# Kernel optimization log

Hardware: AMD Instinct MI355X
Metric: run time of the kernel (lower is better)

## Reference

```python
import jax, jax.numpy as jnp
import numpy as np

N_NODES = 25000
N_EDGES = 400000
FEAT = 128
HID = 64
HEADS = 4
NUM_CLASSES = 2
NUM_GRAPHS = 64


def setup_inputs() -> dict:
    key = jax.random.key(0)
    ks = jax.random.split(key, 16)
    x = jax.random.normal(ks[0], (N_NODES, FEAT), dtype=jnp.float32)
    edge_index = jax.random.randint(ks[1], (2, N_EDGES), 0, N_NODES, dtype=jnp.int32)
    batch = jnp.sort(jax.random.randint(ks[2], (N_NODES,), 0, NUM_GRAPHS, dtype=jnp.int32))
    s = 1.0 / np.sqrt(FEAT)
    sh = 1.0 / np.sqrt(HID)
    shc = 1.0 / np.sqrt(HID * HEADS)
    return {
        "x": x,
        "edge_index": edge_index,
        "batch": batch,
        # conv1: GraphConv(FEAT -> HID): lin_rel (bias) on aggregated neighbors + lin_root (no bias)
        "W1_rel": jax.random.uniform(ks[3], (FEAT, HID), jnp.float32, -s, s),
        "b1": jnp.zeros((HID,), jnp.float32),
        "W1_root": jax.random.uniform(ks[4], (FEAT, HID), jnp.float32, -s, s),
        # conv3: GATConv(HID -> HID, heads=HEADS), concat output [N, HEADS*HID]
        "Wg": jax.random.uniform(ks[5], (HID, HEADS * HID), jnp.float32, -sh, sh),
        "att_src": jax.random.uniform(ks[6], (HEADS, HID), jnp.float32, -sh, sh),
        "att_dst": jax.random.uniform(ks[7], (HEADS, HID), jnp.float32, -sh, sh),
        "bg": jnp.zeros((HEADS * HID,), jnp.float32),
        # conv5: GraphConv(HEADS*HID -> HID)
        "W5_rel": jax.random.uniform(ks[8], (HEADS * HID, HID), jnp.float32, -shc, shc),
        "b5": jnp.zeros((HID,), jnp.float32),
        "W5_root": jax.random.uniform(ks[9], (HEADS * HID, HID), jnp.float32, -shc, shc),
        # fc head
        "W_fc1": jax.random.uniform(ks[10], (HID, HID), jnp.float32, -sh, sh),
        "b_fc1": jnp.zeros((HID,), jnp.float32),
        "W_fc2": jax.random.uniform(ks[11], (HID, NUM_CLASSES), jnp.float32, -sh, sh),
        "b_fc2": jnp.zeros((NUM_CLASSES,), jnp.float32),
    }


def _graph_conv(h, src, dst, W_rel, b, W_root):
    # PyG GraphConv (aggr='add'): out_i = W_rel @ sum_{j->i} h_j + b + W_root @ h_i
    agg = jax.ops.segment_sum(h[src], dst, num_segments=N_NODES)
    return agg @ W_rel + b + h @ W_root


def _gat_conv(h, src, dst, Wg, att_src, att_dst, bg):
    # GATConv with default add_self_loops=True; eval mode (no attn dropout)
    n = h.shape[0]
    loop = jnp.arange(n, dtype=src.dtype)
    si = jnp.concatenate([src, loop])
    di = jnp.concatenate([dst, loop])
    xl = (h @ Wg).reshape(n, HEADS, HID)              # [N, H, C]
    a_s = jnp.sum(xl * att_src, axis=-1)              # [N, H]
    a_d = jnp.sum(xl * att_dst, axis=-1)              # [N, H]
    e = jax.nn.leaky_relu(a_s[si] + a_d[di], 0.2)     # [E', H]
    m = jax.ops.segment_max(e, di, num_segments=n)
    p = jnp.exp(e - m[di])
    denom = jax.ops.segment_sum(p, di, num_segments=n)
    alpha = p / denom[di]                             # segment softmax over incoming edges
    out = jax.ops.segment_sum(alpha[:, :, None] * xl[si], di, num_segments=n)
    return out.reshape(n, HEADS * HID) + bg


def reference(x, edge_index, batch, W1_rel, b1, W1_root, Wg, att_src, att_dst, bg,
              W5_rel, b5, W5_root, W_fc1, b_fc1, W_fc2, b_fc2):
    src, dst = edge_index[0], edge_index[1]
    h = jax.nn.relu(_graph_conv(x, src, dst, W1_rel, b1, W1_root))
    h = jax.nn.relu(_gat_conv(h, src, dst, Wg, att_src, att_dst, bg))
    h = jax.nn.relu(_graph_conv(h, src, dst, W5_rel, b5, W5_root))
    g = jax.ops.segment_sum(h, batch, num_segments=NUM_GRAPHS)   # global_add_pool
    g = jax.nn.relu(g @ W_fc1 + b_fc1)
    return jax.nn.sigmoid(g @ W_fc2 + b_fc2)
```

## Files before the change

### kernel.cpp

```cpp
#include <hip/hip_runtime.h>
#include <math.h>

#define N_NODES 25000
#define N_EDGES 400000
#define FEAT 128
#define HID 64
#define HEADS 4
#define HH 256
#define NUM_GRAPHS 64
#define BUCKET 96

typedef unsigned short ushort_t;
typedef unsigned int uint_t;
typedef __attribute__((ext_vector_type(8))) short short8;
typedef __attribute__((ext_vector_type(4))) float f32x4;

__device__ __forceinline__ float lrelu(float x){ return x > 0.f ? x : 0.2f*x; }

__device__ __forceinline__ ushort_t f2bf(float f){
  uint_t u = __float_as_uint(f);
  return (ushort_t)((u + 0x7fffu + ((u >> 16) & 1u)) >> 16);
}
#define BF_LO(u) __uint_as_float((u) << 16)
#define BF_HI(u) __uint_as_float((u) & 0xffff0000u)

__global__ __launch_bounds__(256) void conv1_gemm(
    const float* __restrict__ X, const float* __restrict__ Wrel,
    const float* __restrict__ Wroot, const float* __restrict__ bias,
    ushort_t* __restrict__ out_rel_b, float* __restrict__ out_root)
{
  const int w    = __builtin_amdgcn_readfirstlane(threadIdx.x >> 6);
  const int lane = threadIdx.x & 63;
  const int m = w >> 1, q = w & 1;
  const float* Wm = (m ? Wroot : Wrel) + (size_t)q*64*HID;
  float wreg[64];
  #pragma unroll
  for (int k = 0; k < 64; k++) wreg[k] = Wm[k*HID + lane];
  __shared__ float part[2][2][8][64];
  const int base = blockIdx.x*8;
  const float* __restrict__ xr = X + (size_t)base*FEAT + q*64;
  float acc[8] = {0,0,0,0,0,0,0,0};
  #pragma unroll
  for (int k = 0; k < 64; k++){
    const float wv = wreg[k];
    #pragma unroll
    for (int i = 0; i < 8; i++) acc[i] += xr[(size_t)i*FEAT + k]*wv;
  }
  #pragma unroll
  for (int i = 0; i < 8; i++) part[m][q][i][lane] = acc[i];
  __syncthreads();
  #pragma unroll
  for (int t = threadIdx.x; t < 1024; t += 256){
    int mm = t >> 9, ii = (t >> 6) & 7, cc = t & 63;
    float v = part[mm][0][ii][cc] + part[mm][1][ii][cc];
    if (mm) out_root[(size_t)(base+ii)*HID + cc] = v + bias[cc];
    else    out_rel_b[(size_t)(base+ii)*HID + cc] = f2bf(v);
  }
}

__global__ __launch_bounds__(512) void conv5_gemm(
    const float* __restrict__ X, const float* __restrict__ Wrel,
    const float* __restrict__ Wroot, const float* __restrict__ bias,
    ushort_t* __restrict__ out_rel_b, float* __restrict__ out_root)
{
  const int w    = __builtin_amdgcn_readfirstlane(threadIdx.x >> 6);
  const int lane = threadIdx.x & 63;
  const int m = w >> 2, q = w & 3;
  const float* Wm = (m ? Wroot : Wrel) + (size_t)q*64*HID;
  float wreg[64];
  #pragma unroll
  for (int k = 0; k < 64; k++) wreg[k] = Wm[k*HID + lane];
  __shared__ float part[2][4][8][64];
  const int base = blockIdx.x*8;
  const float* __restrict__ xr = X + (size_t)base*HH + q*64;
  float acc[8] = {0,0,0,0,0,0,0,0};
  #pragma unroll
  for (int k = 0; k < 64; k++){
    const float wv = wreg[k];
    #pragma unroll
    for (int i = 0; i < 8; i++) acc[i] += xr[(size_t)i*HH + k]*wv;
  }
  #pragma unroll
  for (int i = 0; i < 8; i++) part[m][q][i][lane] = acc[i];
  __syncthreads();
  #pragma unroll
  for (int t = threadIdx.x; t < 1024; t += 512){
    int mm = t >> 9, ii = (t >> 6) & 7, cc = t & 63;
    float v = part[mm][0][ii][cc] + part[mm][1][ii][cc]
            + part[mm][2][ii][cc] + part[mm][3][ii][cc];
    if (mm) out_root[(size_t)(base+ii)*HID + cc] = v + bias[cc];
    else    out_rel_b[(size_t)(base+ii)*HID + cc] = f2bf(v);
  }
}

__global__ __launch_bounds__(256) void k3_prep(
    const float* __restrict__ Wg, ushort_t* __restrict__ wgb)
{
  const int t = threadIdx.x;
  for (int i = 0; i < 64; i++){
    int e = t*64 + i;
    int j = e & 7, lane = (e >> 3) & 63, kt = (e >> 9) & 1, nt = e >> 10;
    int k = kt*32 + (lane >> 4)*8 + j;
    int n = nt*16 + (lane & 15);
    wgb[e] = f2bf(Wg[k*HH + n]);
  }
}

__global__ __launch_bounds__(256) void k3_mfma(
    const ushort_t* __restrict__ h1b, const ushort_t* __restrict__ wgb,
    const float* __restrict__ att_src, const float* __restrict__ att_dst,
    ushort_t* __restrict__ xlb, float* __restrict__ a_s, float* __restrict__ a_d)
{
  const int wid  = __builtin_amdgcn_readfirstlane(threadIdx.x >> 6);
  const int lane = threadIdx.x & 63;
  const int quad = lane >> 4, col = lane & 15;
  const int nb = blockIdx.x*64 + wid*16;
  const ushort_t* arow = h1b + (size_t)(nb + col)*HID + quad*8;
  short8 a0 = *(const short8*)(arow);
  short8 a1 = *(const short8*)(arow + 32);
  float as_acc[4] = {0,0,0,0}, ad_acc[4] = {0,0,0,0};
  #pragma unroll
  for (int nt = 0; nt < 16; nt++){
    short8 b0 = *(const short8*)(wgb + ((size_t)(nt*2+0)*64 + lane)*8);
    short8 b1 = *(const short8*)(wgb + ((size_t)(nt*2+1)*64 + lane)*8);
    f32x4 d = {0.f, 0.f, 0.f, 0.f};
    d = __builtin_amdgcn_mfma_f32_16x16x32_bf16(a0, b0, d, 0, 0, 0);
    d = __builtin_amdgcn_mfma_f32_16x16x32_bf16(a1, b1, d, 0, 0, 0);
    const int h = nt >> 2;
    const float asv = att_src[h*HID + (nt & 3)*16 + col];
    const float adv = att_dst[h*HID + (nt & 3)*16 + col];
    #pragma unroll
    for (int r = 0; r < 4; r++){
      const int node = nb + quad*4 + r;
      if (node < N_NODES)
        xlb[(size_t)node*HH + nt*16 + col] = f2bf(d[r]);
      as_acc[r] += d[r]*asv;
      ad_acc[r] += d[r]*adv;
    }
    if ((nt & 3) == 3){
      #pragma unroll
      for (int r = 0; r < 4; r++){
        float s1 = as_acc[r], s2 = ad_acc[r];
        #pragma unroll
        for (int off = 1; off < 16; off <<= 1){
          s1 += __shfl_xor(s1, off, 64);
          s2 += __shfl_xor(s2, off, 64);
        }
        const int node = nb + quad*4 + r;
        if (col == 0 && node < N_NODES){
          a_s[node*HEADS + h] = s1;
          a_d[node*HEADS + h] = s2;
        }
        as_acc[r] = 0.f; ad_acc[r] = 0.f;
      }
    }
  }
}

__global__ __launch_bounds__(256) void k_fill(const int* __restrict__ src,
                                              const int* __restrict__ dst,
                                              int* __restrict__ cnt,
                                              int* __restrict__ slot)
{
  int e = blockIdx.x*256 + threadIdx.x;
  if (e >= N_EDGES) return;
  int d = dst[e];
  int pos = atomicAdd(&cnt[d], 1);
  if (pos < BUCKET) slot[(size_t)d*BUCKET + pos] = src[e];
}

template<bool BF16OUT>
__global__ __launch_bounds__(256) void k_aggb(
    const int* __restrict__ cnt, const int* __restrict__ slot,
    const ushort_t* __restrict__ featb, const float* __restrict__ root,
    float* __restrict__ outf, ushort_t* __restrict__ outb)
{
  const int node = blockIdx.x*4 + (threadIdx.x >> 6);
  const int lane = threadIdx.x & 63;
  const int* __restrict__ sl = slot + (size_t)node*BUCKET;
  const int deg = min(cnt[node], BUCKET);
  float acc = root[(size_t)node*HID + lane];
  int e = 0;
  for (; e + 4 <= deg; e += 4){
    int sA = sl[e],   sB = sl[e+1];
    int sC = sl[e+2], sD = sl[e+3];
    float xA = BF_LO((uint_t)featb[(size_t)sA*HID + lane]);
    float xB = BF_LO((uint_t)featb[(size_t)sB*HID + lane]);
    float xC = BF_LO((uint_t)featb[(size_t)sC*HID + lane]);
    float xD = BF_LO((uint_t)featb[(size_t)sD*HID + lane]);
    acc += xA; acc += xB; acc += xC; acc += xD;
  }
  for (; e < deg; e++){
    int s = sl[e];
    acc += BF_LO((uint_t)featb[(size_t)s*HID + lane]);
  }
  const float v = fmaxf(acc, 0.f);
  if (BF16OUT) outb[(size_t)node*HID + lane] = f2bf(v);
  else         outf[(size_t)node*HID + lane] = v;
}

__global__ __launch_bounds__(256) void k_gat_node(
    const int* __restrict__ cnt, const int* __restrict__ slot,
    const uint2* __restrict__ xl2,
    const float* __restrict__ a_s, const float* __restrict__ a_d,
    const float* __restrict__ bg, float* __restrict__ h2)
{
  const int node = blockIdx.x*4 + (threadIdx.x >> 6);
  const int lane = threadIdx.x & 63;
  const int h  = lane >> 4;
  const int el = lane & 15;
  const int* __restrict__ sl = slot + (size_t)node*BUCKET;
  const int deg = min(cnt[node], BUCKET);
  const float adh = a_d[node*HEADS + h];
  float acc0=0, acc1=0, acc2=0, acc3=0;
  float dsum = 0.f;
  for (int base = 0; base < deg; base += 16){
    float pme = 0.f; int sme = node;
    const int e = base + el;
    if (e < deg){
      sme = sl[e];
      pme = __expf(lrelu(a_s[sme*HEADS + h] + adh));
    }
    dsum += pme;
    const int nsub = min(16, deg - base);
    int e4 = 0;
    for (; e4 + 2 <= nsub; e4 += 2){
      const int b0 = (lane & 48) + e4;
      const float pA = __shfl(pme, b0, 64);
      const int   sA = __shfl(sme, b0, 64);
      const float pB = __shfl(pme, b0 + 1, 64);
      const int   sB = __shfl(sme, b0 + 1, 64);
      uint2 rA = xl2[(size_t)sA*64 + lane];
      uint2 rB = xl2[(size_t)sB*64 + lane];
      acc0 += pA*BF_LO(rA.x); acc1 += pA*BF_HI(rA.x);
      acc2 += pA*BF_LO(rA.y); acc3 += pA*BF_HI(rA.y);
      acc0 += pB*BF_LO(rB.x); acc1 += pB*BF_HI(rB.x);
      acc2 += pB*BF_LO(rB.y); acc3 += pB*BF_HI(rB.y);
    }
    if (e4 < nsub){
      const int b0 = (lane & 48) + e4;
      const float pA = __shfl(pme, b0, 64);
      const int   sA = __shfl(sme, b0, 64);
      uint2 rA = xl2[(size_t)sA*64 + lane];
      acc0 += pA*BF_LO(rA.x); acc1 += pA*BF_HI(rA.x);
      acc2 += pA*BF_LO(rA.y); acc3 += pA*BF_HI(rA.y);
    }
  }
  #pragma unroll
  for (int off = 1; off < 16; off <<= 1) dsum += __shfl_xor(dsum, off, 64);
  const float pself = __expf(lrelu(a_s[node*HEADS + h] + adh));
  const float inv = 1.f / (dsum + pself);
  uint2 r = xl2[(size_t)node*64 + lane];
  acc0 += pself*BF_LO(r.x); acc1 += pself*BF_HI(r.x);
  acc2 += pself*BF_LO(r.y); acc3 += pself*BF_HI(r.y);
  const int col0 = lane*4;
  float4 o;
  o.x = fmaxf(acc0*inv + bg[col0+0], 0.f);
  o.y = fmaxf(acc1*inv + bg[col0+1], 0.f);
  o.z = fmaxf(acc2*inv + bg[col0+2], 0.f);
  o.w = fmaxf(acc3*inv + bg[col0+3], 0.f);
  ((float4*)(h2 + (size_t)node*HH))[lane] = o;
}

__global__ __launch_bounds__(256) void k_pool(
    const float* __restrict__ h3, const int* __restrict__ batch,
    float* __restrict__ g)
{
  const int w = blockIdx.x*4 + (threadIdx.x >> 6);
  const int j = threadIdx.x & 63;
  int n0 = w*64;
  if (n0 >= N_NODES) return;
  int n1 = min(n0+64, N_NODES);
  float acc = 0.f;
  int cur = batch[n0];
  for (int n = n0; n < n1; n++){
    int b = batch[n];
    if (b != cur){ atomicAdd(&g[cur*HID + j], acc); acc = 0.f; cur = b; }
    acc += h3[n*HID + j];
  }
  atomicAdd(&g[cur*HID + j], acc);
}

__global__ __launch_bounds__(256) void k_head(
    const float* __restrict__ g, const float* __restrict__ W1,
    const float* __restrict__ b1, const float* __restrict__ W2,
    const float* __restrict__ b2, float* __restrict__ out)
{
  __shared__ float gs[NUM_GRAPHS*HID];
  __shared__ float hh[NUM_GRAPHS*HID];
  for (int i = threadIdx.x; i < NUM_GRAPHS*HID; i += 256) gs[i] = g[i];
  __syncthreads();
  for (int t = threadIdx.x; t < NUM_GRAPHS*HID; t += 256){
    int b = t >> 6, j = t & 63;
    float acc = b1[j];
    for (int k = 0; k < HID; k++) acc += gs[b*HID+k]*W1[k*HID+j];
    hh[t] = fmaxf(acc, 0.f);
  }
  __syncthreads();
  for (int t = threadIdx.x; t < NUM_GRAPHS*2; t += 256){
    int b = t >> 1, c = t & 1;
    float acc = b2[c];
    for (int k = 0; k < HID; k++) acc += hh[b*HID+k]*W2[k*2+c];
    out[t] = 1.f / (1.f + __expf(-acc));
  }
}

extern "C" void kernel_launch(void* const* d_in, const int* in_sizes, int n_in,
                              void* d_out, int out_size, void* d_ws, size_t ws_size,
                              hipStream_t stream)
{
  const float* x       = (const float*)d_in[0];
  const int*   ei      = (const int*)d_in[1];
  const int*   batch   = (const int*)d_in[2];
  const float* W1_rel  = (const float*)d_in[3];
  const float* b1      = (const float*)d_in[4];
  const float* W1_root = (const float*)d_in[5];
  const float* Wg      = (const float*)d_in[6];
  const float* att_src = (const float*)d_in[7];
  const float* att_dst = (const float*)d_in[8];
  const float* bg      = (const float*)d_in[9];
  const float* W5_rel  = (const float*)d_in[10];
  const float* b5      = (const float*)d_in[11];
  const float* W5_root = (const float*)d_in[12];
  const float* W_fc1   = (const float*)d_in[13];
  const float* b_fc1   = (const float*)d_in[14];
  const float* W_fc2   = (const float*)d_in[15];
  const float* b_fc2   = (const float*)d_in[16];
  const int* src = ei;
  const int* dst = ei + N_EDGES;

  float* ws    = (float*)d_ws;
  ushort_t* xr_b = (ushort_t*)ws;
  float* hB    = ws +   800000;
  ushort_t* h1b = (ushort_t*)(ws + 2400000);
  ushort_t* xlb = (ushort_t*)(ws + 3201024);
  float* a_s   = ws +  6401024;
  float* a_d   = ws +  6501024;
  float* h2    = ws +  6601024;
  float* g     = ws + 13001024;
  int*   cnt   = (int*)(ws + 13005120);
  ushort_t* wgb = (ushort_t*)(ws + 13040000);
  int*   slot  = (int*)(ws + 13050000);
  float* out   = (float*)d_out;

  hipMemsetAsync(g, 0, (4096 + N_NODES)*sizeof(float), stream);
  k_fill<<<(N_EDGES+255)/256,256,0,stream>>>(src, dst, cnt, slot);
  k3_prep<<<1,256,0,stream>>>(Wg, wgb);

  conv1_gemm<<<N_NODES/8,256,0,stream>>>(x, W1_rel, W1_root, b1, xr_b, hB);
  k_aggb<true><<<N_NODES/4,256,0,stream>>>(cnt, slot, xr_b, hB, nullptr, h1b);

  k3_mfma<<<(N_NODES+63)/64,256,0,stream>>>(h1b, wgb, att_src, att_dst,
                                            xlb, a_s, a_d);
  k_gat_node<<<N_NODES/4,256,0,stream>>>(cnt, slot,
      (const uint2*)xlb, a_s, a_d, bg, h2);

  conv5_gemm<<<N_NODES/8,512,0,stream>>>(h2, W5_rel, W5_root, b5, xr_b, hB);
  k_aggb<false><<<N_NODES/4,256,0,stream>>>(cnt, slot, xr_b, hB, hB, nullptr);

  k_pool<<<(N_NODES/256)+1,256,0,stream>>>(hB, batch, g);
  k_head<<<1,256,0,stream>>>(g, W_fc1, b_fc1, W_fc2, b_fc2, out);
}
```

Measured before the change: 291.6 us.

## Move conv1 and conv5 GEMMs to bf16 MFMA with prepacked weights

Replaces the scalar FP32 conv1 and conv5 GEMMs with bf16 MFMA kernels whose weights are prepacked once, in a single pack kernel that also handles Wg and fuses rel and root into one 128-wide output. The GAT node kernel now writes h2 in bf16, halving the traffic written there and read by conv5. This targets the FMA-bound scalar GEMMs and the FP32 h2 memory traffic, at the cost of lower precision for x, h2 and the weights.

```diff
diff --git a/kernel.cpp b/kernel.cpp
--- a/kernel.cpp
+++ b/kernel.cpp
@@ -24,85 +24,119 @@
 #define BF_LO(u) __uint_as_float((u) << 16)
 #define BF_HI(u) __uint_as_float((u) & 0xffff0000u)
 
-__global__ __launch_bounds__(256) void conv1_gemm(
-    const float* __restrict__ X, const float* __restrict__ Wrel,
-    const float* __restrict__ Wroot, const float* __restrict__ bias,
+__global__ __launch_bounds__(256) void k_pack(
+    const float* __restrict__ W1_rel, const float* __restrict__ W1_root,
+    const float* __restrict__ W5_rel, const float* __restrict__ W5_root,
+    const float* __restrict__ Wg,
+    ushort_t* __restrict__ wc1b, ushort_t* __restrict__ wc5b,
+    ushort_t* __restrict__ wgb)
+{
+  const int e = blockIdx.x*256 + threadIdx.x;
+  {
+    int j=e&7, lane=(e>>3)&63, kc=(e>>9)&3, nt=e>>11;
+    int k = kc*32 + (lane>>4)*8 + j, n = nt*16 + (lane&15);
+    float v = (n < 64) ? W1_rel[k*64 + n] : W1_root[k*64 + n - 64];
+    wc1b[e] = f2bf(v);
+  }
+  {
+    int j=e&7, lane=(e>>3)&63, kt=(e>>9)&1, nt=e>>10;
+    int k = kt*32 + (lane>>4)*8 + j, n = nt*16 + (lane&15);
+    wgb[e] = f2bf(Wg[k*HH + n]);
+  }
+  #pragma unroll
+  for (int e5 = e; e5 < 32768; e5 += 16384){
+    int j=e5&7, lane=(e5>>3)&63, kc=(e5>>9)&7, nt=e5>>12;
+    int k = kc*32 + (lane>>4)*8 + j, n = nt*16 + (lane&15);
+    float v = (n < 64) ? W5_rel[k*64 + n] : W5_root[k*64 + n - 64];
+    wc5b[e5] = f2bf(v);
+  }
+}
+
+__global__ __launch_bounds__(256) void conv1_mfma(
+    const float* __restrict__ X, const ushort_t* __restrict__ wc1b,
+    const float* __restrict__ bias,
     ushort_t* __restrict__ out_rel_b, float* __restrict__ out_root)
 {
-  const int w    = __builtin_amdgcn_readfirstlane(threadIdx.x >> 6);
+  const int wid  = __builtin_amdgcn_readfirstlane(threadIdx.x >> 6);
   const int lane = threadIdx.x & 63;
-  const int m = w >> 1, q = w & 1;
-  const float* Wm = (m ? Wroot : Wrel) + (size_t)q*64*HID;
-  float wreg[64];
-  #pragma unroll
-  for (int k = 0; k < 64; k++) wreg[k] = Wm[k*HID + lane];
-  __shared__ float part[2][2][8][64];
-  const int base = blockIdx.x*8;
-  const float* __restrict__ xr = X + (size_t)base*FEAT + q*64;
-  float acc[8] = {0,0,0,0,0,0,0,0};
-  #pragma unroll
-  for (int k = 0; k < 64; k++){
-    const float wv = wreg[k];
+  const int quad = lane >> 4, col = lane & 15;
+  const int nb = blockIdx.x*64 + wid*16;
+  if (nb >= N_NODES) return;
+  const int row = min(nb + col, N_NODES-1);
+  const float* __restrict__ xr = X + (size_t)row*FEAT + quad*8;
+  short8 a[4];
+  #pragma unroll
+  for (int kc = 0; kc < 4; kc++){
     #pragma unroll
-    for (int i = 0; i < 8; i++) acc[i] += xr[(size_t)i*FEAT + k]*wv;
-  }
-  #pragma unroll
-  for (int i = 0; i < 8; i++) part[m][q][i][lane] = acc[i];
-  __syncthreads();
-  #pragma unroll
-  for (int t = threadIdx.x; t < 1024; t += 256){
-    int mm = t >> 9, ii = (t >> 6) & 7, cc = t & 63;
-    float v = part[mm][0][ii][cc] + part[mm][1][ii][cc];
-    if (mm) out_root[(size_t)(base+ii)*HID + cc] = v + bias[cc];
-    else    out_rel_b[(size_t)(base+ii)*HID + cc] = f2bf(v);
-  }
-}
-
-__global__ __launch_bounds__(512) void conv5_gemm(
-    const float* __restrict__ X, const float* __restrict__ Wrel,
-    const float* __restrict__ Wroot, const float* __restrict__ bias,
+    for (int j = 0; j < 8; j++)
+      ((ushort_t*)&a[kc])[j] = f2bf(xr[kc*32 + j]);
+  }
+  #pragma unroll
+  for (int nt = 0; nt < 8; nt++){
+    f32x4 d = {0.f,0.f,0.f,0.f};
+    #pragma unroll
+    for (int kc = 0; kc < 4; kc++){
+      short8 b = *(const short8*)(wc1b + ((size_t)(nt*4+kc)*64 + lane)*8);
+      d = __builtin_amdgcn_mfma_f32_16x16x32_bf16(a[kc], b, d, 0, 0, 0);
+    }
+    if (nt < 4){
+      #pragma unroll
+      for (int r = 0; r < 4; r++){
+        const int node = nb + quad*4 + r;
+        if (node < N_NODES)
+          out_rel_b[(size_t)node*HID + nt*16 + col] = f2bf(d[r]);
+      }
+    } else {
+      const float bv = bias[(nt-4)*16 + col];
+      #pragma unroll
+      for (int r = 0; r < 4; r++){
+        const int node = nb + quad*4 + r;
+        if (node < N_NODES)
+          out_root[(size_t)node*HID + (nt-4)*16 + col] = d[r] + bv;
+      }
+    }
+  }
+}
+
+__global__ __launch_bounds__(256) void conv5_mfma(
+    const ushort_t* __restrict__ h2b, const ushort_t* __restrict__ wc5b,
+    const float* __restrict__ bias,
     ushort_t* __restrict__ out_rel_b, float* __restrict__ out_root)
 {
-  const int w    = __builtin_amdgcn_readfirstlane(threadIdx.x >> 6);
+  const int wid  = __builtin_amdgcn_readfirstlane(threadIdx.x >> 6);
   const int lane = threadIdx.x & 63;
-  const int m = w >> 2, q = w & 3;
-  const float* Wm = (m ? Wroot : Wrel) + (size_t)q*64*HID;
-  float wreg[64];
-  #pragma unroll
-  for (int k = 0; k < 64; k++) wreg[k] = Wm[k*HID + lane];
-  __shared__ float part[2][4][8][64];
-  const int base = blockIdx.x*8;
-  const float* __restrict__ xr = X + (size_t)base*HH + q*64;
-  float acc[8] = {0,0,0,0,0,0,0,0};
-  #pragma unroll
-  for (int k = 0; k < 64; k++){
-    const float wv = wreg[k];
+  const int quad = lane >> 4, col = lane & 15;
+  const int nb = blockIdx.x*64 + wid*16;
+  if (nb >= N_NODES) return;
+  const ushort_t* __restrict__ arow = h2b + (size_t)(nb + col)*HH + quad*8;
+  short8 a[8];
+  #pragma unroll
+  for (int kc = 0; kc < 8; kc++)
+    a[kc] = *(const short8*)(arow + kc*32);
+  #pragma unroll
+  for (int nt = 0; nt < 8; nt++){
+    f32x4 d = {0.f,0.f,0.f,0.f};
     #pragma unroll
-    for (int i = 0; i < 8; i++) acc[i] += xr[(size_t)i*HH + k]*wv;
-  }
-  #pragma unroll
-  for (int i = 0; i < 8; i++) part[m][q][i][lane] = acc[i];
-  __syncthreads();
-  #pragma unroll
-  for (int t = threadIdx.x; t < 1024; t += 512){
-    int mm = t >> 9, ii = (t >> 6) & 7, cc = t & 63;
-    float v = part[mm][0][ii][cc] + part[mm][1][ii][cc]
-            + part[mm][2][ii][cc] + part[mm][3][ii][cc];
-    if (mm) out_root[(size_t)(base+ii)*HID + cc] = v + bias[cc];
-    else    out_rel_b[(size_t)(base+ii)*HID + cc] = f2bf(v);
-  }
-}
-
-__global__ __launch_bounds__(256) void k3_prep(
-    const float* __restrict__ Wg, ushort_t* __restrict__ wgb)
-{
-  const int t = threadIdx.x;
-  for (int i = 0; i < 64; i++){
-    int e = t*64 + i;
-    int j = e & 7, lane = (e >> 3) & 63, kt = (e >> 9) & 1, nt = e >> 10;
-    int k = kt*32 + (lane >> 4)*8 + j;
-    int n = nt*16 + (lane & 15);
-    wgb[e] = f2bf(Wg[k*HH + n]);
+    for (int kc = 0; kc < 8; kc++){
+      short8 b = *(const short8*)(wc5b + ((size_t)(nt*8+kc)*64 + lane)*8);
+      d = __builtin_amdgcn_mfma_f32_16x16x32_bf16(a[kc], b, d, 0, 0, 0);
+    }
+    if (nt < 4){
+      #pragma unroll
+      for (int r = 0; r < 4; r++){
+        const int node = nb + quad*4 + r;
+        if (node < N_NODES)
+          out_rel_b[(size_t)node*HID + nt*16 + col] = f2bf(d[r]);
+      }
+    } else {
+      const float bv = bias[(nt-4)*16 + col];
+      #pragma unroll
+      for (int r = 0; r < 4; r++){
+        const int node = nb + quad*4 + r;
+        if (node < N_NODES)
+          out_root[(size_t)node*HID + (nt-4)*16 + col] = d[r] + bv;
+      }
+    }
   }
 }
 
@@ -203,7 +237,7 @@
     const int* __restrict__ cnt, const int* __restrict__ slot,
     const uint2* __restrict__ xl2,
     const float* __restrict__ a_s, const float* __restrict__ a_d,
-    const float* __restrict__ bg, float* __restrict__ h2)
+    const float* __restrict__ bg, ushort_t* __restrict__ h2b)
 {
   const int node = blockIdx.x*4 + (threadIdx.x >> 6);
   const int lane = threadIdx.x & 63;
@@ -254,12 +288,14 @@
   acc0 += pself*BF_LO(r.x); acc1 += pself*BF_HI(r.x);
   acc2 += pself*BF_LO(r.y); acc3 += pself*BF_HI(r.y);
   const int col0 = lane*4;
-  float4 o;
-  o.x = fmaxf(acc0*inv + bg[col0+0], 0.f);
-  o.y = fmaxf(acc1*inv + bg[col0+1], 0.f);
-  o.z = fmaxf(acc2*inv + bg[col0+2], 0.f);
-  o.w = fmaxf(acc3*inv + bg[col0+3], 0.f);
-  ((float4*)(h2 + (size_t)node*HH))[lane] = o;
+  const float ox = fmaxf(acc0*inv + bg[col0+0], 0.f);
+  const float oy = fmaxf(acc1*inv + bg[col0+1], 0.f);
+  const float oz = fmaxf(acc2*inv + bg[col0+2], 0.f);
+  const float ow = fmaxf(acc3*inv + bg[col0+3], 0.f);
+  uint2 o;
+  o.x = (uint_t)f2bf(ox) | ((uint_t)f2bf(oy) << 16);
+  o.y = (uint_t)f2bf(oz) | ((uint_t)f2bf(ow) << 16);
+  ((uint2*)(h2b + (size_t)node*HH))[lane] = o;
 }
 
 __global__ __launch_bounds__(256) void k_pool(
@@ -333,29 +369,32 @@
   ushort_t* xr_b = (ushort_t*)ws;
   float* hB    = ws +   800000;
   ushort_t* h1b = (ushort_t*)(ws + 2400000);
-  ushort_t* xlb = (ushort_t*)(ws + 3201024);
-  float* a_s   = ws +  6401024;
-  float* a_d   = ws +  6501024;
-  float* h2    = ws +  6601024;
-  float* g     = ws + 13001024;
-  int*   cnt   = (int*)(ws + 13005120);
-  ushort_t* wgb = (ushort_t*)(ws + 13040000);
-  int*   slot  = (int*)(ws + 13050000);
+  ushort_t* xlb = (ushort_t*)(ws + 3200768);
+  float* a_s   = ws +  6400768;
+  float* a_d   = ws +  6500768;
+  ushort_t* h2b = (ushort_t*)(ws + 6600768);
+  float* g     = ws +  9803840;
+  int*   cnt   = (int*)(ws + 9807936);
+  ushort_t* wc1b = (ushort_t*)(ws + 9833600);
+  ushort_t* wc5b = (ushort_t*)(ws + 9841792);
+  ushort_t* wgb  = (ushort_t*)(ws + 9858176);
+  int*   slot  = (int*)(ws + 9870000);
   float* out   = (float*)d_out;
 
   hipMemsetAsync(g, 0, (4096 + N_NODES)*sizeof(float), stream);
   k_fill<<<(N_EDGES+255)/256,256,0,stream>>>(src, dst, cnt, slot);
-  k3_prep<<<1,256,0,stream>>>(Wg, wgb);
-
-  conv1_gemm<<<N_NODES/8,256,0,stream>>>(x, W1_rel, W1_root, b1, xr_b, hB);
+  k_pack<<<64,256,0,stream>>>(W1_rel, W1_root, W5_rel, W5_root, Wg,
+                              wc1b, wc5b, wgb);
+
+  conv1_mfma<<<(N_NODES+63)/64,256,0,stream>>>(x, wc1b, b1, xr_b, hB);
   k_aggb<true><<<N_NODES/4,256,0,stream>>>(cnt, slot, xr_b, hB, nullptr, h1b);
 
   k3_mfma<<<(N_NODES+63)/64,256,0,stream>>>(h1b, wgb, att_src, att_dst,
                                             xlb, a_s, a_d);
   k_gat_node<<<N_NODES/4,256,0,stream>>>(cnt, slot,
-      (const uint2*)xlb, a_s, a_d, bg, h2);
-
-  conv5_gemm<<<N_NODES/8,512,0,stream>>>(h2, W5_rel, W5_root, b5, xr_b, hB);
+      (const uint2*)xlb, a_s, a_d, bg, h2b);
+
+  conv5_mfma<<<(N_NODES+63)/64,256,0,stream>>>(h2b, wc5b, b5, xr_b, hB);
   k_aggb<false><<<N_NODES/4,256,0,stream>>>(cnt, slot, xr_b, hB, hB, nullptr);
 
   k_pool<<<(N_NODES/256)+1,256,0,stream>>>(hB, batch, g);
```

Measured after the change: 255.1 us. -12.5%, faster.
